# Optimization experiments

Hardware: AMD Instinct MI355X
Metric: run time of the kernel (lower is better)

## Reference

```python
import jax, jax.numpy as jnp
import numpy as np

N_NODES = 100000
N_EDGES = 1000000
D_IN = 64
D_MODEL = 64  # H * D
H = 4
D = D_MODEL // H


def setup_inputs() -> dict:
    key = jax.random.key(0)
    ks = jax.random.split(key, 9)
    nodes = jax.random.normal(ks[0], (N_NODES, D_IN), dtype=jnp.float32)
    senders = jax.random.randint(ks[1], (N_EDGES,), 0, N_NODES, dtype=jnp.int32)
    receivers = jnp.sort(jax.random.randint(ks[2], (N_EDGES,), 0, N_NODES, dtype=jnp.int32))
    s = 1.0 / np.sqrt(D_IN)
    W_qk = jax.random.uniform(ks[3], (D_IN, D_MODEL), jnp.float32, -s, s)
    b_qk = jnp.zeros((D_MODEL,), jnp.float32)
    W_v = jax.random.uniform(ks[4], (D_IN, D_MODEL), jnp.float32, -s, s)
    b_v = jnp.zeros((D_MODEL,), jnp.float32)
    so = 1.0 / np.sqrt(D_MODEL)
    W_out = jax.random.uniform(ks[5], (D_MODEL, D_MODEL), jnp.float32, -so, so)
    b_out = jnp.zeros((D_MODEL,), jnp.float32)
    return {
        'nodes': nodes, 'W_qk': W_qk, 'b_qk': b_qk, 'W_v': W_v, 'b_v': b_v,
        'W_out': W_out, 'b_out': b_out, 'senders': senders, 'receivers': receivers,
    }


def _segment_softmax(logits, segment_ids, num_segments):
    # jraph-style numerically stable segment softmax (segments are sorted)
    maxs = jax.ops.segment_max(logits, segment_ids, num_segments, indices_are_sorted=True)
    e = jnp.exp(logits - maxs[segment_ids])
    z = jax.ops.segment_sum(e, segment_ids, num_segments, indices_are_sorted=True)
    return e / z[segment_ids]


def reference(nodes, W_qk, b_qk, W_v, b_v, W_out, b_out, senders, receivers):
    N = nodes.shape[0]
    # projections: N (H D) -> N H D
    qks = (nodes @ W_qk + b_qk).reshape(N, H, D)
    vs = (nodes @ W_v + b_v).reshape(N, H, D)
    # per-edge QK scores: [E, H]
    scores = jnp.einsum('ehd,ehd->eh', qks[receivers], qks[senders])
    attn = _segment_softmax(scores, receivers, N)
    # weighted message scatter: [E,H,D] -> [N, H*D]
    messages = (attn[..., None] * vs[senders]).reshape(-1, H * D)
    ctx = jax.ops.segment_sum(messages, receivers, N, indices_are_sorted=True)
    out = ctx @ W_out + b_out
    return out, attn
```

## Files before the change

### kernel.cpp

```cpp
#include <hip/hip_runtime.h>
#include <math.h>


typedef _Float16 h2 __attribute__((ext_vector_type(2)));
typedef _Float16 half8 __attribute__((ext_vector_type(8)));
typedef float floatx4 __attribute__((ext_vector_type(4)));

#define SP_ROW 136

__global__ __launch_bounds__(256) void mhga_prep(
    const float* __restrict__ Wqk, const float* __restrict__ Wv,
    _Float16* __restrict__ Wt,
    const int* __restrict__ receivers, int* __restrict__ row_ptr,
    int N, int E)
{
    if ((int)blockIdx.x < 32) {
        const int idx = blockIdx.x * 256 + threadIdx.x;
        const int n = idx >> 6, k = idx & 63;
        const float w = (n < 64) ? Wqk[k * 64 + n] : Wv[k * 64 + (n - 64)];
        Wt[idx] = (_Float16)w;
        return;
    }
    const int n = (blockIdx.x - 32) * 256 + threadIdx.x;
    if (n > N) return;
    int lo = 0, hi = E;
    while (lo < hi) {
        const int mid = (lo + hi) >> 1;
        if (receivers[mid] < n) lo = mid + 1; else hi = mid;
    }
    row_ptr[n] = lo;
}

__global__ __launch_bounds__(256) void mhga_proj(
    const float* __restrict__ X, const _Float16* __restrict__ Wt,
    const float* __restrict__ bqk, const float* __restrict__ bv,
    unsigned char* __restrict__ packed, int N)
{
    __shared__ __align__(16) _Float16 sP[64 * SP_ROW];
    const int t = threadIdx.x;
    const int w = t >> 6, lane = t & 63;
    const int ln = lane & 15, quad = lane >> 4;
    const int m0 = blockIdx.x * 64;

    const int arow = min(m0 + w * 16 + ln, N - 1);
    const float* xr = X + (size_t)arow * 64;
    const float4 xa = *(const float4*)(xr + quad * 8);
    const float4 xb = *(const float4*)(xr + quad * 8 + 4);
    const float4 xc = *(const float4*)(xr + 32 + quad * 8);
    const float4 xd = *(const float4*)(xr + 32 + quad * 8 + 4);
    const half8 a0 = { (_Float16)xa.x, (_Float16)xa.y, (_Float16)xa.z,
                       (_Float16)xa.w, (_Float16)xb.x, (_Float16)xb.y,
                       (_Float16)xb.z, (_Float16)xb.w };
    const half8 a1 = { (_Float16)xc.x, (_Float16)xc.y, (_Float16)xc.z,
                       (_Float16)xc.w, (_Float16)xd.x, (_Float16)xd.y,
                       (_Float16)xd.z, (_Float16)xd.w };

    floatx4 acc[8];
#pragma unroll
    for (int tt = 0; tt < 8; ++tt) {
        const _Float16* wrow = Wt + (tt * 16 + ln) * 64;
        const half8 b0 = *(const half8*)(wrow + quad * 8);
        const half8 b1 = *(const half8*)(wrow + 32 + quad * 8);
        floatx4 c = {0.f, 0.f, 0.f, 0.f};
        c = __builtin_amdgcn_mfma_f32_16x16x32_f16(a0, b0, c, 0, 0, 0);
        c = __builtin_amdgcn_mfma_f32_16x16x32_f16(a1, b1, c, 0, 0, 0);
        acc[tt] = c;
    }

#pragma unroll
    for (int tt = 0; tt < 8; ++tt) {
        const float bt = (tt < 4) ? bqk[tt * 16 + ln] : bv[(tt - 4) * 16 + ln];
        const int j = (tt & 3) * 16 + ln;
        const int fidx = (j >> 2) * 8 + ((tt < 4) ? 0 : 4) + (j & 3);
#pragma unroll
        for (int r = 0; r < 4; ++r) {
            const int lrow = w * 16 + quad * 4 + r;
            sP[lrow * SP_ROW + fidx] = (_Float16)(acc[tt][r] + bt);
        }
    }

    const int crow = w * 16 + (lane >> 2);
    const int grow = m0 + crow;
    if (grow < N) {
        const _Float16* src = sP + crow * SP_ROW + (lane & 3) * 32;
        unsigned char* dst = packed + (size_t)grow * 256 + (lane & 3) * 64;
#pragma unroll
        for (int c = 0; c < 4; ++c)
            *(uint4*)(dst + c * 16) = *(const uint4*)(src + c * 8);
    }
}

__global__ __launch_bounds__(256) void mhga_attn(
    const unsigned char* __restrict__ packed,
    const int* __restrict__ senders, const int* __restrict__ row_ptr,
    const float* __restrict__ Wout, const float* __restrict__ bout,
    float* __restrict__ out, float* __restrict__ attn_out, int N)
{
    __shared__ float sW[64 * 64];
    __shared__ float sCtx[4][64];
    __shared__ float sAtt[4][256];
    const int t = threadIdx.x;
#pragma unroll
    for (int i = t * 4; i < 4096; i += 1024)
        *(float4*)(sW + i) = *(const float4*)(Wout + i);

    const int wave = t >> 6, lane = t & 63;
    const int g = lane >> 4, tl = lane & 15;
    const float bo = bout[lane];
    __syncthreads();

    for (int n = blockIdx.x * 4 + wave; n < N; n += gridDim.x * 4) {
        const int e0 = row_ptr[n];
        const int e1 = row_ptr[n + 1];
        const int cnt = e1 - e0;

        float l = 0.f;
        float4 ctx = make_float4(0.f, 0.f, 0.f, 0.f);
        const uint4 qpk = *(const uint4*)(packed + (size_t)n * 256 + tl * 16);
        const h2 q0 = __builtin_bit_cast(h2, qpk.x);
        const h2 q1 = __builtin_bit_cast(h2, qpk.y);

        if (cnt <= 64) {
            int sid = 0;
            if (e0 + lane < e1) sid = senders[e0 + lane];
            const int iters = (cnt + 3) >> 2;
            for (int i = 0; i < iters; ++i) {
                const int idx = i * 4 + g;
                const int s = __shfl(sid, idx, 64);
                const uint4 pk =
                    *(const uint4*)(packed + (size_t)s * 256 + tl * 16);
                const h2 k0 = __builtin_bit_cast(h2, pk.x);
                const h2 k1 = __builtin_bit_cast(h2, pk.y);
                const h2 v0 = __builtin_bit_cast(h2, pk.z);
                const h2 v1 = __builtin_bit_cast(h2, pk.w);
                float d = __builtin_amdgcn_fdot2(q0, k0, 0.f, false);
                d = __builtin_amdgcn_fdot2(q1, k1, d, false);
                d += __shfl_xor(d, 1, 64);
                d += __shfl_xor(d, 2, 64);
                float p = __expf(d);
                p = (idx < cnt) ? p : 0.f;
                if ((tl & 3) == 0)
                    sAtt[wave][idx * 4 + (tl >> 2)] = p;
                l += p;
                ctx.x = fmaf(p, (float)v0.x, ctx.x);
                ctx.y = fmaf(p, (float)v0.y, ctx.y);
                ctx.z = fmaf(p, (float)v1.x, ctx.z);
                ctx.w = fmaf(p, (float)v1.y, ctx.w);
            }
        } else {
            for (int base = e0; base < e1; base += 64) {
                const int c2 = min(64, e1 - base);
                int sid = 0;
                if (base + lane < e1) sid = senders[base + lane];
                const int it2 = (c2 + 3) >> 2;
                for (int i = 0; i < it2; ++i) {
                    const int idx = i * 4 + g;
                    const int s = __shfl(sid, idx, 64);
                    if (idx < c2) {
                        const uint4 pk =
                            *(const uint4*)(packed + (size_t)s * 256 + tl * 16);
                        const h2 k0 = __builtin_bit_cast(h2, pk.x);
                        const h2 k1 = __builtin_bit_cast(h2, pk.y);
                        const h2 v0 = __builtin_bit_cast(h2, pk.z);
                        const h2 v1 = __builtin_bit_cast(h2, pk.w);
                        float d = __builtin_amdgcn_fdot2(q0, k0, 0.f, false);
                        d = __builtin_amdgcn_fdot2(q1, k1, d, false);
                        d += __shfl_xor(d, 1, 64);
                        d += __shfl_xor(d, 2, 64);
                        const float p = __expf(d);
                        if ((tl & 3) == 0)
                            attn_out[(size_t)(base + idx) * 4 + (tl >> 2)] = p;
                        l += p;
                        ctx.x = fmaf(p, (float)v0.x, ctx.x);
                        ctx.y = fmaf(p, (float)v0.y, ctx.y);
                        ctx.z = fmaf(p, (float)v1.x, ctx.z);
                        ctx.w = fmaf(p, (float)v1.y, ctx.w);
                    }
                }
            }
        }

#pragma unroll
        for (int mask = 16; mask <= 32; mask <<= 1) {
            l     += __shfl_xor(l, mask, 64);
            ctx.x += __shfl_xor(ctx.x, mask, 64);
            ctx.y += __shfl_xor(ctx.y, mask, 64);
            ctx.z += __shfl_xor(ctx.z, mask, 64);
            ctx.w += __shfl_xor(ctx.w, mask, 64);
        }
        const float inv = (l > 0.f) ? (1.f / l) : 0.f;
        if (g == 0) {
            *(float4*)(&sCtx[wave][tl * 4]) =
                make_float4(ctx.x * inv, ctx.y * inv, ctx.z * inv, ctx.w * inv);
        }

        const float lh = __shfl(l, (lane & 3) << 2, 64);
        const float invl = (lh > 0.f) ? (1.f / lh) : 0.f;
        if (cnt <= 64) {
            const int cnt4 = cnt * 4;
            for (int f = lane; f < cnt4; f += 64)
                attn_out[e0 * 4 + f] = sAtt[wave][f] * invl;
        } else {
            __builtin_amdgcn_s_waitcnt(0x0F70);
            volatile const float* vp = attn_out;
            for (int f = e0 * 4 + lane; f < e1 * 4; f += 64)
                attn_out[f] = vp[f] * invl;
        }

        float acc = bo;
#pragma unroll
        for (int k = 0; k < 64; k += 4) {
            const float4 c = *(const float4*)(&sCtx[wave][k]);
            acc = fmaf(c.x, sW[(k + 0) * 64 + lane], acc);
            acc = fmaf(c.y, sW[(k + 1) * 64 + lane], acc);
            acc = fmaf(c.z, sW[(k + 2) * 64 + lane], acc);
            acc = fmaf(c.w, sW[(k + 3) * 64 + lane], acc);
        }
        out[(size_t)n * 64 + lane] = acc;
    }
}

extern "C" void kernel_launch(void* const* d_in, const int* in_sizes, int n_in,
                              void* d_out, int out_size, void* d_ws, size_t ws_size,
                              hipStream_t stream) {
    const float* nodes   = (const float*)d_in[0];
    const float* W_qk    = (const float*)d_in[1];
    const float* b_qk    = (const float*)d_in[2];
    const float* W_v     = (const float*)d_in[3];
    const float* b_v     = (const float*)d_in[4];
    const float* W_out   = (const float*)d_in[5];
    const float* b_out   = (const float*)d_in[6];
    const int* senders   = (const int*)d_in[7];
    const int* receivers = (const int*)d_in[8];

    const int N = in_sizes[0] / 64;
    const int E = in_sizes[7];

    float* out      = (float*)d_out;
    float* attn_out = out + (size_t)N * 64;

    unsigned char* packed = (unsigned char*)d_ws;
    int*   rowp = (int*)(packed + (size_t)N * 256);
    float* p_ws = (float*)(rowp + (((N + 1) + 3) & ~3));
    _Float16* Wt = (_Float16*)(p_ws + (size_t)E * 4);

    const int RB = (N + 1 + 255) / 256;
    mhga_prep<<<32 + RB, 256, 0, stream>>>(W_qk, W_v, Wt, receivers, rowp, N, E);
    mhga_proj<<<(N + 63) / 64, 256, 0, stream>>>(nodes, Wt, b_qk, b_v,
                                                 packed, N);
    mhga_attn<<<1792, 256, 0, stream>>>(packed, senders, rowp,
                                        W_out, b_out, out, attn_out, N);
}
```

Measured before the change: 191.0 us.

## Software-pipeline node metadata and neighbor gathers in attention kernel

Prefetches the next node's row_ptr, query vector and sender ids while the current node is processed, and double-buffers the per-edge K/V gather so the load for the next group of edges is issued before the current one is consumed. It also reuses the sAtt shared buffer for the context vector, splits the output projection into four independent accumulators, sets launch_bounds occupancy to 8 and raises the grid to 2048 blocks. The aim is to hide global-memory latency on the gather-bound loop, at the cost of more registers and some extra redundant loads on the last iteration.

```diff
diff --git a/kernel.cpp b/kernel.cpp
--- a/kernel.cpp
+++ b/kernel.cpp
@@ -90,14 +90,13 @@
     }
 }
 
-__global__ __launch_bounds__(256) void mhga_attn(
+__global__ __launch_bounds__(256, 8) void mhga_attn(
     const unsigned char* __restrict__ packed,
     const int* __restrict__ senders, const int* __restrict__ row_ptr,
     const float* __restrict__ Wout, const float* __restrict__ bout,
     float* __restrict__ out, float* __restrict__ attn_out, int N)
 {
     __shared__ float sW[64 * 64];
-    __shared__ float sCtx[4][64];
     __shared__ float sAtt[4][256];
     const int t = threadIdx.x;
 #pragma unroll
@@ -109,26 +108,40 @@
     const float bo = bout[lane];
     __syncthreads();
 
-    for (int n = blockIdx.x * 4 + wave; n < N; n += gridDim.x * 4) {
-        const int e0 = row_ptr[n];
-        const int e1 = row_ptr[n + 1];
+    const int stride = gridDim.x * 4;
+    int n = blockIdx.x * 4 + wave;
+
+    const int nf = min(n, N - 1);
+    int e0 = row_ptr[nf];
+    int e1 = row_ptr[nf + 1];
+    uint4 qpk = *(const uint4*)(packed + (size_t)nf * 256 + tl * 16);
+    int sid = 0;
+    if (e0 + lane < e1) sid = senders[e0 + lane];
+
+    while (n < N) {
+        const int nn = n + stride;
+        const int nc = min(nn, N - 1);
+        const int e0n = row_ptr[nc];
+        const int e1n = row_ptr[nc + 1];
+        const uint4 qn = *(const uint4*)(packed + (size_t)nc * 256 + tl * 16);
+
         const int cnt = e1 - e0;
-
+        const h2 q0 = __builtin_bit_cast(h2, qpk.x);
+        const h2 q1 = __builtin_bit_cast(h2, qpk.y);
         float l = 0.f;
         float4 ctx = make_float4(0.f, 0.f, 0.f, 0.f);
-        const uint4 qpk = *(const uint4*)(packed + (size_t)n * 256 + tl * 16);
-        const h2 q0 = __builtin_bit_cast(h2, qpk.x);
-        const h2 q1 = __builtin_bit_cast(h2, qpk.y);
 
         if (cnt <= 64) {
-            int sid = 0;
-            if (e0 + lane < e1) sid = senders[e0 + lane];
             const int iters = (cnt + 3) >> 2;
+            int s = __shfl(sid, g, 64);
+            uint4 pk = *(const uint4*)(packed + (size_t)s * 256 + tl * 16);
             for (int i = 0; i < iters; ++i) {
+                uint4 pkn = pk;
+                if (i + 1 < iters) {
+                    const int s2 = __shfl(sid, (i + 1) * 4 + g, 64);
+                    pkn = *(const uint4*)(packed + (size_t)s2 * 256 + tl * 16);
+                }
                 const int idx = i * 4 + g;
-                const int s = __shfl(sid, idx, 64);
-                const uint4 pk =
-                    *(const uint4*)(packed + (size_t)s * 256 + tl * 16);
                 const h2 k0 = __builtin_bit_cast(h2, pk.x);
                 const h2 k1 = __builtin_bit_cast(h2, pk.y);
                 const h2 v0 = __builtin_bit_cast(h2, pk.z);
@@ -146,16 +159,17 @@
                 ctx.y = fmaf(p, (float)v0.y, ctx.y);
                 ctx.z = fmaf(p, (float)v1.x, ctx.z);
                 ctx.w = fmaf(p, (float)v1.y, ctx.w);
+                pk = pkn;
             }
         } else {
             for (int base = e0; base < e1; base += 64) {
                 const int c2 = min(64, e1 - base);
-                int sid = 0;
-                if (base + lane < e1) sid = senders[base + lane];
+                int sid2 = 0;
+                if (base + lane < e1) sid2 = senders[base + lane];
                 const int it2 = (c2 + 3) >> 2;
                 for (int i = 0; i < it2; ++i) {
                     const int idx = i * 4 + g;
-                    const int s = __shfl(sid, idx, 64);
+                    const int s = __shfl(sid2, idx, 64);
                     if (idx < c2) {
                         const uint4 pk =
                             *(const uint4*)(packed + (size_t)s * 256 + tl * 16);
@@ -189,10 +203,6 @@
             ctx.w += __shfl_xor(ctx.w, mask, 64);
         }
         const float inv = (l > 0.f) ? (1.f / l) : 0.f;
-        if (g == 0) {
-            *(float4*)(&sCtx[wave][tl * 4]) =
-                make_float4(ctx.x * inv, ctx.y * inv, ctx.z * inv, ctx.w * inv);
-        }
 
         const float lh = __shfl(l, (lane & 3) << 2, 64);
         const float invl = (lh > 0.f) ? (1.f / lh) : 0.f;
@@ -207,16 +217,42 @@
                 attn_out[f] = vp[f] * invl;
         }
 
-        float acc = bo;
-#pragma unroll
-        for (int k = 0; k < 64; k += 4) {
-            const float4 c = *(const float4*)(&sCtx[wave][k]);
-            acc = fmaf(c.x, sW[(k + 0) * 64 + lane], acc);
-            acc = fmaf(c.y, sW[(k + 1) * 64 + lane], acc);
-            acc = fmaf(c.z, sW[(k + 2) * 64 + lane], acc);
-            acc = fmaf(c.w, sW[(k + 3) * 64 + lane], acc);
-        }
-        out[(size_t)n * 64 + lane] = acc;
+        int sidn = 0;
+        if (e0n + lane < e1n) sidn = senders[e0n + lane];
+
+        if (g == 0) {
+            *(float4*)(&sAtt[wave][tl * 4]) =
+                make_float4(ctx.x * inv, ctx.y * inv, ctx.z * inv, ctx.w * inv);
+        }
+
+        const float* sCtx = &sAtt[wave][0];
+        float a0 = bo, a1 = 0.f, a2 = 0.f, a3 = 0.f;
+#pragma unroll
+        for (int k = 0; k < 64; k += 16) {
+            const float4 c0 = *(const float4*)(sCtx + k);
+            const float4 c1 = *(const float4*)(sCtx + k + 4);
+            const float4 c2 = *(const float4*)(sCtx + k + 8);
+            const float4 c3 = *(const float4*)(sCtx + k + 12);
+            a0 = fmaf(c0.x, sW[(k + 0) * 64 + lane], a0);
+            a0 = fmaf(c0.y, sW[(k + 1) * 64 + lane], a0);
+            a0 = fmaf(c0.z, sW[(k + 2) * 64 + lane], a0);
+            a0 = fmaf(c0.w, sW[(k + 3) * 64 + lane], a0);
+            a1 = fmaf(c1.x, sW[(k + 4) * 64 + lane], a1);
+            a1 = fmaf(c1.y, sW[(k + 5) * 64 + lane], a1);
+            a1 = fmaf(c1.z, sW[(k + 6) * 64 + lane], a1);
+            a1 = fmaf(c1.w, sW[(k + 7) * 64 + lane], a1);
+            a2 = fmaf(c2.x, sW[(k + 8) * 64 + lane], a2);
+            a2 = fmaf(c2.y, sW[(k + 9) * 64 + lane], a2);
+            a2 = fmaf(c2.z, sW[(k + 10) * 64 + lane], a2);
+            a2 = fmaf(c2.w, sW[(k + 11) * 64 + lane], a2);
+            a3 = fmaf(c3.x, sW[(k + 12) * 64 + lane], a3);
+            a3 = fmaf(c3.y, sW[(k + 13) * 64 + lane], a3);
+            a3 = fmaf(c3.z, sW[(k + 14) * 64 + lane], a3);
+            a3 = fmaf(c3.w, sW[(k + 15) * 64 + lane], a3);
+        }
+        out[(size_t)n * 64 + lane] = (a0 + a1) + (a2 + a3);
+
+        n = nn; e0 = e0n; e1 = e1n; qpk = qn; sid = sidn;
     }
 }
 
@@ -241,13 +277,13 @@
 
     unsigned char* packed = (unsigned char*)d_ws;
     int*   rowp = (int*)(packed + (size_t)N * 256);
-    float* p_ws = (float*)(rowp + (((N + 1) + 3) & ~3));
-    _Float16* Wt = (_Float16*)(p_ws + (size_t)E * 4);
+    float* spare = (float*)(rowp + (((N + 1) + 3) & ~3));
+    _Float16* Wt = (_Float16*)(spare + (size_t)E * 4);
 
     const int RB = (N + 1 + 255) / 256;
     mhga_prep<<<32 + RB, 256, 0, stream>>>(W_qk, W_v, Wt, receivers, rowp, N, E);
     mhga_proj<<<(N + 63) / 64, 256, 0, stream>>>(nodes, Wt, b_qk, b_v,
                                                  packed, N);
-    mhga_attn<<<1792, 256, 0, stream>>>(packed, senders, rowp,
+    mhga_attn<<<2048, 256, 0, stream>>>(packed, senders, rowp,
                                         W_out, b_out, out, attn_out, N);
 }
```

New measurement: 203.6 us. +6.6%, slower.
